# Kernel optimization log

Hardware: AMD Instinct MI355X
Metric: run time of the kernel (lower is better)

## Reference

```python
import jax, jax.numpy as jnp
import numpy as np

N_HEADS = 16
SCALE = 8.0  # sqrt(inner_dim // n_heads) = sqrt(64), scale='inv_sqrt'


def setup_inputs() -> dict:
    key = jax.random.key(0)
    k1, k2, k3, k4 = jax.random.split(key, 4)
    b, n, d_model, inner = 8, 2048, 1024, 1024
    x = jax.random.normal(k1, (b, n, d_model), dtype=jnp.float32)
    Wqkv = jax.random.normal(k2, (3 * inner, d_model), dtype=jnp.float32) * (1.0 / np.sqrt(d_model))
    Wproj = jax.random.normal(k3, (d_model, inner), dtype=jnp.float32) * (1.0 / np.sqrt(inner))
    bproj = jax.random.normal(k4, (d_model,), dtype=jnp.float32) * 0.01
    return {"x": x, "Wqkv": Wqkv, "Wproj": Wproj, "bproj": bproj}


def reference(x, Wqkv, Wproj, bproj):
    b, n, _ = x.shape
    qkv = jnp.einsum('bnm,fm->bnf', x, Wqkv)          # [b, n, 3*inner]
    qkv = qkv.reshape(b, n, N_HEADS, -1)              # [b, n, h, 3*dh] (einops 'b n (h d)')
    dh = qkv.shape[3] // 3
    q, k, v = qkv[..., :dh], qkv[..., dh:2 * dh], qkv[..., 2 * dh:]
    # Faithful to source: q @ k.transpose(-1,-2) on [b,n,h,dh] -> scores over HEADS, [b,n,h,h]
    scores = jnp.einsum('bnhd,bngd->bnhg', q, k) / SCALE
    attn = jax.nn.softmax(scores, axis=-1)            # softmax over last head axis
    out = jnp.einsum('bnhg,bngd->bnhd', attn, v)      # [b, n, h, dh]
    out = out.reshape(b, n, -1)                       # [b, n, inner]
    return jnp.einsum('bni,mi->bnm', out, Wproj) + bproj
```

## Files before the change

kernel.cpp:

```cpp
#include <hip/hip_runtime.h>
#include <stdint.h>

typedef __bf16 bf16_t;
typedef __bf16 bf16x8 __attribute__((ext_vector_type(8)));
typedef float f32x4 __attribute__((ext_vector_type(4)));

__device__ __forceinline__ void gload_lds16(const void* g, void* l) {
  __builtin_amdgcn_global_load_lds(
      (const __attribute__((address_space(1))) uint32_t*)g,
      (__attribute__((address_space(3))) uint32_t*)l, 16, 0, 0);
}

__global__ void cast_f32_bf16(const float* __restrict__ in,
                              bf16_t* __restrict__ out, int n4) {
  int i = blockIdx.x * blockDim.x + threadIdx.x;
  int stride = gridDim.x * blockDim.x;
  for (int idx = i; idx < n4; idx += stride) {
    float4 v = reinterpret_cast<const float4*>(in)[idx];
    union { bf16_t b[4]; uint2 u; } pk;
    pk.b[0] = (bf16_t)v.x; pk.b[1] = (bf16_t)v.y;
    pk.b[2] = (bf16_t)v.z; pk.b[3] = (bf16_t)v.w;
    reinterpret_cast<uint2*>(out)[idx] = pk.u;
  }
}

template <bool BF16_OUT>
__global__ __launch_bounds__(512, 2)
void gemm_pipe(const bf16_t* __restrict__ A, const bf16_t* __restrict__ B,
               void* __restrict__ Cout, const float* __restrict__ bias,
               int N) {
  constexpr int K = 1024, NT = 32;
  __shared__ bf16_t Al[4][256 * 32];
  __shared__ bf16_t Bl[4][256 * 32];

  const int tid = threadIdx.x;
  const int l = tid & 63, w = tid >> 6;
  const int wm = w >> 2, wn = w & 3;

  const int bid = blockIdx.x;
  const int xcd = bid & 7;
  const int idx = bid >> 3;
  const int bx = xcd * 8 + (idx & 7);
  const int by = idx >> 3;
  const int m0 = bx * 256, n0 = by * 256;

  const int ra = tid >> 2;
  const int ca = ((tid & 3) ^ (ra & 3)) * 8;
  const bf16_t* pA0 = A + (size_t)(m0 +   0 + ra) * K + ca;
  const bf16_t* pA1 = A + (size_t)(m0 + 128 + ra) * K + ca;
  const bf16_t* pB0 = B + (size_t)(n0 +   0 + ra) * K + ca;
  const bf16_t* pB1 = B + (size_t)(n0 + 128 + ra) * K + ca;
  const int wb = w * 512;

#define STAGE(t_, s_) do {                          \
    const int kt_ = (t_) * 32;                      \
    gload_lds16(pA0 + kt_, &Al[s_][wb]);            \
    gload_lds16(pA1 + kt_, &Al[s_][4096 + wb]);     \
    gload_lds16(pB0 + kt_, &Bl[s_][wb]);            \
    gload_lds16(pB1 + kt_, &Bl[s_][4096 + wb]);     \
  } while (0)

  const int abase = (wm * 128 + (l & 15)) * 32;
  const int bbase = (wn * 64 + (l & 15)) * 32;
  const int ck = (((l >> 4) ^ (l & 3))) * 8;

  f32x4 acc[8][4] = {};

  STAGE(0, 0);
  STAGE(1, 1);
  STAGE(2, 2);

  int slot = 0;
  for (int t = 0; t < NT; ++t) {
    if (t < NT - 2)       asm volatile("s_waitcnt vmcnt(8)" ::: "memory");
    else if (t == NT - 2) asm volatile("s_waitcnt vmcnt(4)" ::: "memory");
    else                  asm volatile("s_waitcnt vmcnt(0)" ::: "memory");
    __builtin_amdgcn_s_barrier();
    asm volatile("" ::: "memory");
    if (t + 3 < NT) {
      int s3 = (slot + 3) & 3;
      STAGE(t + 3, s3);
    }
    const bf16_t* As = Al[slot];
    const bf16_t* Bs = Bl[slot];
    bf16x8 af[8], bfr[4];
#pragma unroll
    for (int i = 0; i < 8; ++i)
      af[i] = *reinterpret_cast<const bf16x8*>(&As[abase + i * 512 + ck]);
#pragma unroll
    for (int j = 0; j < 4; ++j)
      bfr[j] = *reinterpret_cast<const bf16x8*>(&Bs[bbase + j * 512 + ck]);
    __builtin_amdgcn_s_setprio(1);
#pragma unroll
    for (int i = 0; i < 8; ++i)
#pragma unroll
      for (int j = 0; j < 4; ++j)
        acc[i][j] = __builtin_amdgcn_mfma_f32_16x16x32_bf16(af[i], bfr[j],
                                                            acc[i][j], 0, 0, 0);
    __builtin_amdgcn_s_setprio(0);
    slot = (slot + 1) & 3;
  }
#undef STAGE

  const int r0 = m0 + wm * 128 + (l >> 4) * 4;
  const int c0 = n0 + wn * 64 + (l & 15);
  if (BF16_OUT) {
    bf16_t* C = (bf16_t*)Cout;
#pragma unroll
    for (int i = 0; i < 8; ++i)
#pragma unroll
      for (int j = 0; j < 4; ++j)
#pragma unroll
        for (int r = 0; r < 4; ++r)
          C[(size_t)(r0 + i * 16 + r) * N + (c0 + j * 16)] = (bf16_t)acc[i][j][r];
  } else {
    float* C = (float*)Cout;
#pragma unroll
    for (int i = 0; i < 8; ++i)
#pragma unroll
      for (int j = 0; j < 4; ++j)
#pragma unroll
        for (int r = 0; r < 4; ++r)
          C[(size_t)(r0 + i * 16 + r) * N + (c0 + j * 16)] =
              acc[i][j][r] + bias[c0 + j * 16];
  }
}

__global__ __launch_bounds__(256)
void attn_heads(const bf16_t* __restrict__ qkv, bf16_t* __restrict__ out) {
  __shared__ float s[4][3072];
  const int w = threadIdx.x >> 6, l = threadIdx.x & 63;
  const size_t t = (size_t)blockIdx.x * 4 + w;
  const bf16_t* src = qkv + t * 3072;
#pragma unroll
  for (int i = 0; i < 6; ++i) {
    int f = (i * 64 + l) * 8;
    bf16x8 v = *reinterpret_cast<const bf16x8*>(&src[f]);
#pragma unroll
    for (int jj = 0; jj < 8; ++jj) s[w][f + jj] = (float)v[jj];
  }
  __syncthreads();

  const int h = l >> 2, ss = l & 3;
  float qr[16];
  const float* qb = &s[w][h * 192 + ss * 16];
#pragma unroll
  for (int d = 0; d < 16; ++d) qr[d] = qb[d];

  float sc[16];
#pragma unroll
  for (int g = 0; g < 16; ++g) {
    const float* kk = &s[w][g * 192 + 64 + ss * 16];
    float p = 0.f;
#pragma unroll
    for (int d = 0; d < 16; ++d) p += qr[d] * kk[d];
    p += __shfl_xor(p, 1);
    p += __shfl_xor(p, 2);
    sc[g] = p * 0.125f;
  }
  float m = sc[0];
#pragma unroll
  for (int g = 1; g < 16; ++g) m = fmaxf(m, sc[g]);
  float sum = 0.f;
#pragma unroll
  for (int g = 0; g < 16; ++g) { sc[g] = __expf(sc[g] - m); sum += sc[g]; }
  float inv = 1.f / sum;

  float o[16] = {};
#pragma unroll
  for (int g = 0; g < 16; ++g) {
    float a = sc[g] * inv;
    const float* vv = &s[w][g * 192 + 128 + ss * 16];
#pragma unroll
    for (int d = 0; d < 16; ++d) o[d] += a * vv[d];
  }
  union { bf16_t b[16]; uint4 u[2]; } pk;
#pragma unroll
  for (int d = 0; d < 16; ++d) pk.b[d] = (bf16_t)o[d];
  uint4* dst = reinterpret_cast<uint4*>(out + t * 1024 + h * 64 + ss * 16);
  dst[0] = pk.u[0];
  dst[1] = pk.u[1];
}

extern "C" void kernel_launch(void* const* d_in, const int* in_sizes, int n_in,
                              void* d_out, int out_size, void* d_ws, size_t ws_size,
                              hipStream_t stream) {
  const float* x     = (const float*)d_in[0];
  const float* Wqkv  = (const float*)d_in[1];
  const float* Wproj = (const float*)d_in[2];
  const float* bproj = (const float*)d_in[3];
  float* out = (float*)d_out;

  const int M = 8 * 2048;
  const int DM = 1024;
  const int F = 3072;

  char* ws = (char*)d_ws;
  bf16_t* xb     = (bf16_t*)ws;  ws += (size_t)M * DM * 2;
  bf16_t* wqkvb  = (bf16_t*)ws;  ws += (size_t)F * DM * 2;
  bf16_t* wprojb = (bf16_t*)ws;  ws += (size_t)DM * DM * 2;
  bf16_t* qkvb   = (bf16_t*)ws;  ws += (size_t)M * F * 2;
  bf16_t* attnb  = (bf16_t*)ws;

  cast_f32_bf16<<<2048, 256, 0, stream>>>(x, xb, M * DM / 4);
  cast_f32_bf16<<<512, 256, 0, stream>>>(Wqkv, wqkvb, F * DM / 4);
  cast_f32_bf16<<<256, 256, 0, stream>>>(Wproj, wprojb, DM * DM / 4);

  gemm_pipe<true><<<(M / 256) * (F / 256), 512, 0, stream>>>(
      xb, wqkvb, (void*)qkvb, nullptr, F);

  attn_heads<<<M / 4, 256, 0, stream>>>(qkvb, attnb);

  gemm_pipe<false><<<(M / 256) * (DM / 256), 512, 0, stream>>>(
      attnb, wprojb, (void*)out, bproj, DM);
}
```

Measured before the change: 244.0 us.

## Load pre-swizzled B operand directly to registers, shrink A LDS pipeline to double buffer

Adds a weight-transform kernel that casts weights to bf16 and lays them out in MFMA fragment order. The GEMM can then load B fragments straight from global memory into registers, bypassing LDS. The A operand keeps going through LDS but is cut from a 4-stage to a 2-stage ring, with a changed swizzle and one barrier per k-step. This removes B traffic through LDS and cuts LDS footprint, at the cost of a shallower prefetch depth and B loads that go through registers with latency exposed across only one tile.

```diff
diff --git a/kernel.cpp b/kernel.cpp
--- a/kernel.cpp
+++ b/kernel.cpp
@@ -24,83 +24,106 @@
   }
 }
 
+__global__ void wtransform(const float* __restrict__ W, bf16_t* __restrict__ Wp,
+                           int N, int K) {
+  int wid = (blockIdx.x * blockDim.x + threadIdx.x) >> 6;
+  int l = threadIdx.x & 63;
+  int nb = (N / 16) * (K / 32);
+  if (wid >= nb) return;
+  int n16 = wid / (K / 32), k32 = wid % (K / 32);
+  const float* src = W + (size_t)(n16 * 16 + (l & 15)) * K + k32 * 32 + (l >> 4) * 8;
+  float4 v0 = *reinterpret_cast<const float4*>(src);
+  float4 v1 = *reinterpret_cast<const float4*>(src + 4);
+  union { bf16_t b[8]; uint4 u; } pk;
+  pk.b[0] = (bf16_t)v0.x; pk.b[1] = (bf16_t)v0.y;
+  pk.b[2] = (bf16_t)v0.z; pk.b[3] = (bf16_t)v0.w;
+  pk.b[4] = (bf16_t)v1.x; pk.b[5] = (bf16_t)v1.y;
+  pk.b[6] = (bf16_t)v1.z; pk.b[7] = (bf16_t)v1.w;
+  *reinterpret_cast<uint4*>(Wp + (size_t)wid * 512 + l * 8) = pk.u;
+}
+
 template <bool BF16_OUT>
 __global__ __launch_bounds__(512, 2)
-void gemm_pipe(const bf16_t* __restrict__ A, const bf16_t* __restrict__ B,
-               void* __restrict__ Cout, const float* __restrict__ bias,
-               int N) {
+void gemm_bd(const bf16_t* __restrict__ A, const bf16_t* __restrict__ Bp,
+             void* __restrict__ Cout, const float* __restrict__ bias, int N) {
   constexpr int K = 1024, NT = 32;
-  __shared__ bf16_t Al[4][256 * 32];
-  __shared__ bf16_t Bl[4][256 * 32];
+  __shared__ bf16_t Al[2][256 * 32];
 
   const int tid = threadIdx.x;
   const int l = tid & 63, w = tid >> 6;
   const int wm = w >> 2, wn = w & 3;
 
   const int bid = blockIdx.x;
-  const int xcd = bid & 7;
-  const int idx = bid >> 3;
+  const int xcd = bid & 7, idx = bid >> 3;
   const int bx = xcd * 8 + (idx & 7);
   const int by = idx >> 3;
   const int m0 = bx * 256, n0 = by * 256;
 
   const int ra = tid >> 2;
-  const int ca = ((tid & 3) ^ (ra & 3)) * 8;
-  const bf16_t* pA0 = A + (size_t)(m0 +   0 + ra) * K + ca;
+  const int ca = ((tid & 3) ^ ((tid >> 3) & 3)) * 8;
+  const bf16_t* pA0 = A + (size_t)(m0 + ra) * K + ca;
   const bf16_t* pA1 = A + (size_t)(m0 + 128 + ra) * K + ca;
-  const bf16_t* pB0 = B + (size_t)(n0 +   0 + ra) * K + ca;
-  const bf16_t* pB1 = B + (size_t)(n0 + 128 + ra) * K + ca;
   const int wb = w * 512;
 
-#define STAGE(t_, s_) do {                          \
-    const int kt_ = (t_) * 32;                      \
-    gload_lds16(pA0 + kt_, &Al[s_][wb]);            \
-    gload_lds16(pA1 + kt_, &Al[s_][4096 + wb]);     \
-    gload_lds16(pB0 + kt_, &Bl[s_][wb]);            \
-    gload_lds16(pB1 + kt_, &Bl[s_][4096 + wb]);     \
+#define ST_A(t_, s_) do { const int kt_ = (t_) * 32;   \
+    gload_lds16(pA0 + kt_, &Al[s_][wb]);               \
+    gload_lds16(pA1 + kt_, &Al[s_][4096 + wb]); } while (0)
+
+  const int abase = (wm * 128 + (l & 15)) * 32;
+  const int ck = ((l >> 4) ^ ((l >> 1) & 3)) * 8;
+
+#define RDA(s_) do { const bf16_t* As_ = Al[s_];                                  \
+    _Pragma("unroll") for (int i = 0; i < 8; ++i)                                 \
+      af[i] = *reinterpret_cast<const bf16x8*>(&As_[abase + i * 512 + ck]);       \
   } while (0)
 
-  const int abase = (wm * 128 + (l & 15)) * 32;
-  const int bbase = (wn * 64 + (l & 15)) * 32;
-  const int ck = (((l >> 4) ^ (l & 3))) * 8;
+  const bf16_t* Bw = Bp + ((size_t)(n0 / 16 + wn * 4) * 32) * 512 + (size_t)l * 8;
+
+#define BLOAD(dst, t_) do {                                                       \
+    _Pragma("unroll") for (int j = 0; j < 4; ++j)                                 \
+      dst[j] = *reinterpret_cast<const bf16x8*>(Bw + j * 16384 + (t_) * 512);     \
+  } while (0)
+
+#define MM32(bf_)                                                                 \
+    __builtin_amdgcn_s_setprio(1);                                                \
+    _Pragma("unroll") for (int i = 0; i < 8; ++i)                                 \
+    _Pragma("unroll") for (int j = 0; j < 4; ++j)                                 \
+      acc[i][j] = __builtin_amdgcn_mfma_f32_16x16x32_bf16(                        \
+          af[i], bf_[j], acc[i][j], 0, 0, 0);                                     \
+    __builtin_amdgcn_s_setprio(0);
+
+#define BARF() do { asm volatile("" ::: "memory");  \
+    __builtin_amdgcn_s_barrier();                   \
+    asm volatile("" ::: "memory"); } while (0)
+
+#define TILE(t_, BC, BN_) do {                                                    \
+    if ((t_) + 1 < NT) { ST_A((t_) + 1, ((t_) + 1) & 1); BLOAD(BN_, (t_) + 1); }  \
+    RDA((t_) & 1);                                                                \
+    MM32(BC);                                                                     \
+    if ((t_) + 1 < NT) {                                                          \
+      asm volatile("s_waitcnt vmcnt(4)" ::: "memory");                            \
+      BARF();                                                                     \
+    }                                                                             \
+  } while (0)
 
   f32x4 acc[8][4] = {};
-
-  STAGE(0, 0);
-  STAGE(1, 1);
-  STAGE(2, 2);
-
-  int slot = 0;
-  for (int t = 0; t < NT; ++t) {
-    if (t < NT - 2)       asm volatile("s_waitcnt vmcnt(8)" ::: "memory");
-    else if (t == NT - 2) asm volatile("s_waitcnt vmcnt(4)" ::: "memory");
-    else                  asm volatile("s_waitcnt vmcnt(0)" ::: "memory");
-    __builtin_amdgcn_s_barrier();
-    asm volatile("" ::: "memory");
-    if (t + 3 < NT) {
-      int s3 = (slot + 3) & 3;
-      STAGE(t + 3, s3);
-    }
-    const bf16_t* As = Al[slot];
-    const bf16_t* Bs = Bl[slot];
-    bf16x8 af[8], bfr[4];
-#pragma unroll
-    for (int i = 0; i < 8; ++i)
-      af[i] = *reinterpret_cast<const bf16x8*>(&As[abase + i * 512 + ck]);
-#pragma unroll
-    for (int j = 0; j < 4; ++j)
-      bfr[j] = *reinterpret_cast<const bf16x8*>(&Bs[bbase + j * 512 + ck]);
-    __builtin_amdgcn_s_setprio(1);
-#pragma unroll
-    for (int i = 0; i < 8; ++i)
-#pragma unroll
-      for (int j = 0; j < 4; ++j)
-        acc[i][j] = __builtin_amdgcn_mfma_f32_16x16x32_bf16(af[i], bfr[j],
-                                                            acc[i][j], 0, 0, 0);
-    __builtin_amdgcn_s_setprio(0);
-    slot = (slot + 1) & 3;
-  }
-#undef STAGE
+  bf16x8 af[8], bcur[4], bnext[4];
+
+  ST_A(0, 0);
+  BLOAD(bcur, 0);
+  asm volatile("s_waitcnt vmcnt(4)" ::: "memory");
+  BARF();
+
+  for (int t = 0; t < NT; t += 2) {
+    TILE(t, bcur, bnext);
+    TILE(t + 1, bnext, bcur);
+  }
+#undef ST_A
+#undef RDA
+#undef BLOAD
+#undef MM32
+#undef BARF
+#undef TILE
 
   const int r0 = m0 + wm * 128 + (l >> 4) * 4;
   const int c0 = n0 + wn * 64 + (l & 15);
@@ -197,20 +220,20 @@
 
   char* ws = (char*)d_ws;
   bf16_t* xb     = (bf16_t*)ws;  ws += (size_t)M * DM * 2;
-  bf16_t* wqkvb  = (bf16_t*)ws;  ws += (size_t)F * DM * 2;
-  bf16_t* wprojb = (bf16_t*)ws;  ws += (size_t)DM * DM * 2;
+  bf16_t* wqkvp  = (bf16_t*)ws;  ws += (size_t)F * DM * 2;
+  bf16_t* wprojp = (bf16_t*)ws;  ws += (size_t)DM * DM * 2;
   bf16_t* qkvb   = (bf16_t*)ws;  ws += (size_t)M * F * 2;
   bf16_t* attnb  = (bf16_t*)ws;
 
   cast_f32_bf16<<<2048, 256, 0, stream>>>(x, xb, M * DM / 4);
-  cast_f32_bf16<<<512, 256, 0, stream>>>(Wqkv, wqkvb, F * DM / 4);
-  cast_f32_bf16<<<256, 256, 0, stream>>>(Wproj, wprojb, DM * DM / 4);
-
-  gemm_pipe<true><<<(M / 256) * (F / 256), 512, 0, stream>>>(
-      xb, wqkvb, (void*)qkvb, nullptr, F);
+  wtransform<<<(F / 16) * (DM / 32) / 4, 256, 0, stream>>>(Wqkv, wqkvp, F, DM);
+  wtransform<<<(DM / 16) * (DM / 32) / 4, 256, 0, stream>>>(Wproj, wprojp, DM, DM);
+
+  gemm_bd<true><<<(M / 256) * (F / 256), 512, 0, stream>>>(
+      xb, wqkvp, (void*)qkvb, nullptr, F);
 
   attn_heads<<<M / 4, 256, 0, stream>>>(qkvb, attnb);
 
-  gemm_pipe<false><<<(M / 256) * (DM / 256), 512, 0, stream>>>(
-      attnb, wprojb, (void*)out, bproj, DM);
-}
+  gemm_bd<false><<<(M / 256) * (DM / 256), 512, 0, stream>>>(
+      attnb, wprojp, (void*)out, bproj, DM);
+}
```

Measured after the change: 212.4 us. -13.0%, faster.
